# Kernel optimization log

Hardware: AMD Instinct MI355X
Metric: run time of the kernel (lower is better)

## Reference

```python
import jax, jax.numpy as jnp
import numpy as np

N_HEADS = 4
N_HIDDEN = 256  # out_features with concat=False
SLOPE = 0.1
NEG_INF = -9e15


def setup_inputs() -> dict:
    key = jax.random.key(0)
    k1, k2, k3, k4 = jax.random.split(key, 4)
    N, F_IN = 4096, 512
    h = jax.random.normal(k1, (N, F_IN), dtype=jnp.float32)
    adj_mat = jax.random.randint(k2, (N, N), 0, 2, dtype=jnp.int32)
    # xavier_normal gain=1.414
    W = jax.random.normal(k3, (F_IN, N_HIDDEN * N_HEADS), dtype=jnp.float32) * (
        1.414 * np.sqrt(2.0 / (F_IN + N_HIDDEN * N_HEADS)))
    a = jax.random.normal(k4, (N_HEADS, 2 * N_HIDDEN, 1), dtype=jnp.float32) * (
        1.414 * np.sqrt(2.0 / (2 * N_HIDDEN + 1)))
    return {"h": h, "adj_mat": adj_mat, "W": W, "a": a}


def reference(h, adj_mat, W, a):
    N = h.shape[0]
    # [N, H*D] -> [H, N, D]
    ht = (h @ W).reshape(N, N_HEADS, N_HIDDEN).transpose(1, 0, 2)
    lr = jax.nn.leaky_relu(ht, SLOPE)
    # additive attention: a split into source/target halves
    src = jnp.einsum('hnd,hd->hn', lr, a[:, :N_HIDDEN, 0])   # [H, N]
    tgt = jnp.einsum('hnd,hd->hn', lr, a[:, N_HIDDEN:, 0])   # [H, N]
    e = src[:, :, None] + tgt[:, None, :]                    # [H, N, N]
    e = jnp.where(adj_mat > 0, e, NEG_INF)
    attn = jax.nn.softmax(e, axis=-1)
    out = jnp.einsum('hnm,hmd->hnd', attn, ht)               # [H, N, D]
    return out.mean(axis=0)                                  # concat=False -> mean over heads
```

## Files before the change

### kernel.cpp

```cpp
#include <hip/hip_runtime.h>

#define N_NODES 4096
#define F_IN 512
#define NHID 256
#define HD 1024
#define NPAD 1152

typedef _Float16 half8 __attribute__((ext_vector_type(8)));
typedef _Float16 half4 __attribute__((ext_vector_type(4)));
typedef float floatx4 __attribute__((ext_vector_type(4)));
typedef float float4v __attribute__((ext_vector_type(4)));
typedef int int4v __attribute__((ext_vector_type(4)));
typedef unsigned int uint4v __attribute__((ext_vector_type(4)));

__device__ __forceinline__ float bf2f(unsigned short u) {
  union { unsigned int i; float f; } x; x.i = ((unsigned int)u) << 16; return x.f;
}

__device__ __forceinline__ void async_copy16(const void* g, void* l) {
  __builtin_amdgcn_global_load_lds((const __attribute__((address_space(1))) void*)g,
                                   (__attribute__((address_space(3))) void*)l, 16, 0, 0);
}

__global__ void detect_kernel(const unsigned short* __restrict__ hbits, int* __restrict__ flag) {
  const int t = threadIdx.x;
  int cnt = 0;
  for (int i = t; i < 1024; i += 256) {
    int e = (hbits[i] >> 7) & 0xFF;
    cnt += (e >= 115 && e <= 135) ? 1 : 0;
  }
  __shared__ int red[256];
  red[t] = cnt; __syncthreads();
  for (int s = 128; s > 0; s >>= 1) { if (t < s) red[t] += red[t + s]; __syncthreads(); }
  if (t == 0) flag[0] = (red[0] >= 900) ? 1 : 0;
}

template <typename OutT>
__device__ __forceinline__ void gemm_core(
    const _Float16* __restrict__ A, const _Float16* __restrict__ BT,
    OutT* __restrict__ C, int K, int ldc, int klen, long csz,
    int lin, int nbx, int nby, int total,
    _Float16* __restrict__ sA, _Float16* __restrict__ sB)
{
  int tile = ((total & 7) == 0) ? ((lin & 7) * (total >> 3) + (lin >> 3)) : lin;
  const int n_idx = tile % nbx;
  const int rem   = tile / nbx;
  const int m_idx = rem % nby;
  const int kz    = rem / nby;

  const int n0 = n_idx * 128;
  const int m0 = m_idx * 128;
  const int kbeg = kz * klen;
  const int kend = kbeg + klen;
  OutT* Cz = C + (long)kz * csz;

  const int t = threadIdx.x;
  const int w = t >> 6;
  const int lane = t & 63;
  const int wm = (w >> 1) << 6;
  const int wn = (w & 1) << 6;

  floatx4 acc[4][4] = {};

  const int l4 = lane >> 2;
  const int kksw = (((lane & 3) ^ ((lane >> 2) & 3)) << 3);
  const int c0 = w << 1;

  const _Float16* gA = A + (long)m0 * K;
  const _Float16* gBT = BT + (long)n0 * K;

  const int rsw = (((lane >> 4) ^ (lane & 3)) << 3);
  const int rA = wm + (lane & 15);
  const int rB = wn + (lane & 15);

  auto STAGE = [&](int buf, int k0) {
#pragma unroll
    for (int p = 0; p < 2; ++p) {
      const int c = c0 + p;
      const int row = c * 16 + l4;
      async_copy16(gA + (long)row * K + k0 + kksw, &sA[buf * 4096 + c * 512 + lane * 8]);
      async_copy16(gBT + (long)row * K + k0 + kksw, &sB[buf * 4096 + c * 512 + lane * 8]);
    }
  };

  STAGE(0, kbeg);
  __syncthreads();

  int cur = 0;
  for (int k0 = kbeg; k0 < kend; k0 += 32) {
    if (k0 + 32 < kend) STAGE(cur ^ 1, k0 + 32);

    half8 af[4], bf[4];
#pragma unroll
    for (int i = 0; i < 4; ++i)
      af[i] = *(const half8*)&sA[cur * 4096 + (rA + i * 16) * 32 + rsw];
#pragma unroll
    for (int i = 0; i < 4; ++i)
      bf[i] = *(const half8*)&sB[cur * 4096 + (rB + i * 16) * 32 + rsw];
#pragma unroll
    for (int i = 0; i < 4; ++i)
#pragma unroll
      for (int j = 0; j < 4; ++j)
        acc[i][j] = __builtin_amdgcn_mfma_f32_16x16x32_f16(af[i], bf[j], acc[i][j], 0, 0, 0);

    __syncthreads();
    cur ^= 1;
  }

  const int q4 = (lane >> 4) << 2;
#pragma unroll
  for (int i = 0; i < 4; ++i) {
#pragma unroll
    for (int j = 0; j < 4; ++j) {
      const int gr = m0 + wm + i * 16 + q4;
      const int gc = n0 + wn + j * 16 + (lane & 15);
#pragma unroll
      for (int r = 0; r < 4; ++r)
        Cz[(long)(gr + r) * ldc + gc] = (OutT)acc[i][j][r];
    }
  }
}

template <typename OutT>
__global__ __launch_bounds__(256) void gemm_bt(
    const _Float16* __restrict__ A, const _Float16* __restrict__ BT,
    OutT* __restrict__ C, int K, int ldc, int klen, long csz)
{
  __shared__ _Float16 sA[2 * 128 * 32];
  __shared__ _Float16 sB[2 * 128 * 32];
  const int nbx = gridDim.x, nby = gridDim.y;
  const int total = nbx * nby * gridDim.z;
  const int lin = blockIdx.x + nbx * (blockIdx.y + nby * blockIdx.z);
  gemm_core<OutT>(A, BT, C, K, ldc, klen, csz, lin, nbx, nby, total, sA, sB);
}

__global__ __launch_bounds__(256) void fused_ht_cvt_kernel(
    const _Float16* __restrict__ hF, const _Float16* __restrict__ WT,
    _Float16* __restrict__ ht, const int* __restrict__ adj,
    _Float16* __restrict__ adjF)
{
  __shared__ _Float16 sA[2 * 128 * 32];
  __shared__ _Float16 sB[2 * 128 * 32];
  const int b = blockIdx.x;
  if (b < 256) {
    gemm_core<_Float16>(hF, WT, ht, F_IN, HD, F_IN, 0, b, 8, 32, 256, sA, sB);
  } else {
    const int i = (b - 256) * 256 + threadIdx.x;
    int4v A = ((const int4v*)adj)[2 * i];
    int4v B = ((const int4v*)adj)[2 * i + 1];
    half8 o;
#pragma unroll
    for (int e = 0; e < 4; ++e) {
      o[e]     = (_Float16)(A[e] > 0 ? 1.0f : 0.0f);
      o[4 + e] = (_Float16)(B[e] > 0 ? 1.0f : 0.0f);
    }
    ((half8*)adjF)[i] = o;
  }
}

__global__ void cvt_h_kernel(const void* __restrict__ in, _Float16* __restrict__ out,
                             const int* __restrict__ flag, int n8) {
  int i = blockIdx.x * 256 + threadIdx.x;
  if (i >= n8) return;
  half8 o;
  if (*flag) {
    union { uint4v v; unsigned short s[8]; } u;
    u.v = ((const uint4v*)in)[i];
#pragma unroll
    for (int e = 0; e < 8; ++e) o[e] = (_Float16)bf2f(u.s[e]);
  } else {
    const float4v* f = (const float4v*)in + 2 * i;
    float4v x0 = f[0], x1 = f[1];
#pragma unroll
    for (int e = 0; e < 4; ++e) { o[e] = (_Float16)x0[e]; o[4 + e] = (_Float16)x1[e]; }
  }
  ((half8*)out)[i] = o;
}

__global__ void cvt_a_kernel(const void* __restrict__ a, float* __restrict__ aF,
                             const int* __restrict__ flag) {
  const int t = threadIdx.x;
  const int bf = *flag;
#pragma unroll
  for (int e = 0; e < 8; ++e) {
    int idx = t * 8 + e;
    aF[idx] = bf ? bf2f(((const unsigned short*)a)[idx]) : ((const float*)a)[idx];
  }
}

__global__ void transpose_w_kernel(const void* __restrict__ W, _Float16* __restrict__ WT,
                                   const int* __restrict__ flag) {
  __shared__ _Float16 tile[64][72];
  const int k0 = blockIdx.x * 64, n0 = blockIdx.y * 64;
  const int t = threadIdx.x, r = t >> 3, c = t & 7;
  const int bf = *flag;
#pragma unroll
  for (int q = 0; q < 2; ++q) {
    int k = r + q * 32;
    half8 v;
    if (bf) {
      union { uint4v vv; unsigned short s[8]; } u;
      u.vv = *(const uint4v*)&((const unsigned short*)W)[(long)(k0 + k) * HD + n0 + c * 8];
#pragma unroll
      for (int e = 0; e < 8; ++e) v[e] = (_Float16)bf2f(u.s[e]);
    } else {
      const float4v* f = (const float4v*)&((const float*)W)[(long)(k0 + k) * HD + n0 + c * 8];
      float4v x0 = f[0], x1 = f[1];
#pragma unroll
      for (int e = 0; e < 4; ++e) { v[e] = (_Float16)x0[e]; v[4 + e] = (_Float16)x1[e]; }
    }
    *(half8*)&tile[k][c * 8] = v;
  }
  __syncthreads();
#pragma unroll
  for (int q = 0; q < 2; ++q) {
    int n = r + q * 32;
    half8 o;
#pragma unroll
    for (int e = 0; e < 8; ++e) o[e] = tile[c * 8 + e][n];
    *(half8*)&WT[(long)(n0 + n) * F_IN + k0 + c * 8] = o;
  }
}

__global__ void tgt_kernel(const _Float16* __restrict__ ht, const float* __restrict__ aF,
                           float* __restrict__ tgt) {
  const int i = blockIdx.x;
  const int t = threadIdx.x, h = t >> 6, lane = t & 63;
  half4 v = *(const half4*)&ht[(long)i * HD + h * NHID + lane * 4];
  float4v av = *(const float4v*)&aF[h * 512 + NHID + lane * 4];
  float s = 0.f;
#pragma unroll
  for (int e = 0; e < 4; ++e) {
    float x = (float)v[e];
    x = x > 0.f ? x : 0.1f * x;
    s += x * av[e];
  }
#pragma unroll
  for (int o = 32; o > 0; o >>= 1) s += __shfl_down(s, o);
  if (lane == 0) tgt[h * N_NODES + i] = s;
}

__global__ void maxexp_kernel(const float* __restrict__ tgt, float* __restrict__ wbuf,
                              _Float16* __restrict__ VT) {
  const int h = blockIdx.x, t = threadIdx.x;
  const float* row = tgt + h * N_NODES;
  float4v v[4];
  float m = -3.0e38f;
#pragma unroll
  for (int q = 0; q < 4; ++q) {
    v[q] = *(const float4v*)&row[(t + q * 256) * 4];
#pragma unroll
    for (int e = 0; e < 4; ++e) m = fmaxf(m, v[q][e]);
  }
#pragma unroll
  for (int o = 32; o > 0; o >>= 1) m = fmaxf(m, __shfl_down(m, o));
  __shared__ float red[4];
  if ((t & 63) == 0) red[t >> 6] = m;
  __syncthreads();
  m = fmaxf(fmaxf(red[0], red[1]), fmaxf(red[2], red[3]));
#pragma unroll
  for (int q = 0; q < 4; ++q) {
    const int j0 = (t + q * 256) * 4;
    float4v wv;
#pragma unroll
    for (int e = 0; e < 4; ++e) wv[e] = __expf(v[q][e] - m);
    *(float4v*)&wbuf[h * N_NODES + j0] = wv;
    half4 hv;
#pragma unroll
    for (int e = 0; e < 4; ++e) hv[e] = (_Float16)wv[e];
    *(half4*)&VT[(long)(HD + h) * N_NODES + j0] = hv;
  }
}

__global__ void scaled_transpose_kernel(const _Float16* __restrict__ ht, const float* __restrict__ wbuf,
                                        _Float16* __restrict__ VT) {
  __shared__ _Float16 tile[64][72];
  const int j0 = blockIdx.x * 64, n0 = blockIdx.y * 64;
  const int t = threadIdx.x, r = t >> 3, c = t & 7;
#pragma unroll
  for (int q = 0; q < 2; ++q) {
    int j = r + q * 32;
    *(half8*)&tile[j][c * 8] = *(const half8*)&ht[(long)(j0 + j) * HD + n0 + c * 8];
  }
  __syncthreads();
  const int h = n0 >> 8;
  const float* wrow = wbuf + h * N_NODES + j0;
#pragma unroll
  for (int q = 0; q < 2; ++q) {
    int n = r + q * 32;
    half8 o;
#pragma unroll
    for (int e = 0; e < 8; ++e) {
      int j = c * 8 + e;
      o[e] = (_Float16)(wrow[j] * (float)tile[j][n]);
    }
    *(half8*)&VT[(long)(n0 + n) * N_NODES + j0 + c * 8] = o;
  }
}

__global__ void epilogue_kernel(const float* __restrict__ S, float* __restrict__ out, int ns) {
  const int i = blockIdx.x, d = threadIdx.x;
  const long SZ = (long)N_NODES * NPAD;
  float num[4] = {0.f, 0.f, 0.f, 0.f};
  float den[4] = {0.f, 0.f, 0.f, 0.f};
  for (int z = 0; z < ns; ++z) {
    const float* row = S + z * SZ + (long)i * NPAD;
#pragma unroll
    for (int h = 0; h < 4; ++h) {
      num[h] += row[h * NHID + d];
      den[h] += row[HD + h];
    }
  }
  float r = 0.f;
#pragma unroll
  for (int h = 0; h < 4; ++h) r += num[h] / den[h];
  out[(long)i * NHID + d] = 0.25f * r;
}

extern "C" void kernel_launch(void* const* d_in, const int* in_sizes, int n_in,
                              void* d_out, int out_size, void* d_ws, size_t ws_size,
                              hipStream_t stream) {
  const void* h = nullptr; const int* adj = nullptr; const void* W = nullptr; const void* a = nullptr;
  for (int i = 0; i < n_in; ++i) {
    switch (in_sizes[i]) {
      case 2097152:  h   = d_in[i]; break;
      case 16777216: adj = (const int*)d_in[i]; break;
      case 524288:   W   = d_in[i]; break;
      case 2048:     a   = d_in[i]; break;
      default: break;
    }
  }
  float* out = (float*)d_out;

  char* ws = (char*)d_ws;
  const size_t OFF_ADJF = 0;
  const size_t OFF_VT   = 33554432;
  const size_t OFF_TGT  = OFF_VT + 9437184;
  const size_t OFF_WBUF = OFF_TGT + 65536;
  const size_t OFF_M    = OFF_WBUF + 65536;
  const size_t OFF_AF   = OFF_M + 256;
  const size_t OFF_X    = OFF_AF + 8192;
  const size_t SPART    = 18874368;

  int ns = 1;
  if      (ws_size >= OFF_X + 4 * SPART) ns = 4;
  else if (ws_size >= OFF_X + 2 * SPART) ns = 2;
  if (ws_size < OFF_X + SPART || !h || !adj || !W || !a) return;

  _Float16* adjF = (_Float16*)(ws + OFF_ADJF);
  _Float16* VT   = (_Float16*)(ws + OFF_VT);
  float*    tgt  = (float*)(ws + OFF_TGT);
  float*    wbuf = (float*)(ws + OFF_WBUF);
  int*      flag = (int*)(ws + OFF_M + 32);
  float*    aF   = (float*)(ws + OFF_AF);
  _Float16* hF = (_Float16*)(ws + OFF_X);
  _Float16* WT = (_Float16*)(ws + OFF_X + 4194304);
  _Float16* ht = (_Float16*)(ws + OFF_X + 5242880);
  float*    S  = (float*)(ws + OFF_X);

  detect_kernel<<<1, 256, 0, stream>>>((const unsigned short*)h, flag);
  cvt_h_kernel<<<1024, 256, 0, stream>>>(h, hF, flag, 262144);
  cvt_a_kernel<<<1, 256, 0, stream>>>(a, aF, flag);
  transpose_w_kernel<<<dim3(8, 16), 256, 0, stream>>>(W, WT, flag);
  fused_ht_cvt_kernel<<<8448, 256, 0, stream>>>(hF, WT, ht, adj, adjF);
  tgt_kernel<<<4096, 256, 0, stream>>>(ht, aF, tgt);
  maxexp_kernel<<<4, 256, 0, stream>>>(tgt, wbuf, VT);
  scaled_transpose_kernel<<<dim3(64, 16), 256, 0, stream>>>(ht, wbuf, VT);
  gemm_bt<float><<<dim3(9, 32, ns), 256, 0, stream>>>(adjF, VT, S, N_NODES, NPAD,
                                                      N_NODES / ns, (long)N_NODES * NPAD);
  epilogue_kernel<<<4096, 256, 0, stream>>>(S, out, ns);
}
```

Baseline: 212.1 us.

## Triple-buffer GEMM LDS staging with explicit vmcnt waits and drop swizzle

```diff
diff --git a/kernel.cpp b/kernel.cpp
--- a/kernel.cpp
+++ b/kernel.cpp
@@ -51,7 +51,6 @@
   const int n0 = n_idx * 128;
   const int m0 = m_idx * 128;
   const int kbeg = kz * klen;
-  const int kend = kbeg + klen;
   OutT* Cz = C + (long)kz * csz;
 
   const int t = threadIdx.x;
@@ -63,48 +62,61 @@
   floatx4 acc[4][4] = {};
 
   const int l4 = lane >> 2;
-  const int kksw = (((lane & 3) ^ ((lane >> 2) & 3)) << 3);
+  const int kk = (lane & 3) << 3;
   const int c0 = w << 1;
 
   const _Float16* gA = A + (long)m0 * K;
   const _Float16* gBT = BT + (long)n0 * K;
 
-  const int rsw = (((lane >> 4) ^ (lane & 3)) << 3);
+  const int koff = (lane >> 4) << 3;
   const int rA = wm + (lane & 15);
   const int rB = wn + (lane & 15);
+
+  const int nt = klen >> 5;
 
   auto STAGE = [&](int buf, int k0) {
 #pragma unroll
     for (int p = 0; p < 2; ++p) {
       const int c = c0 + p;
       const int row = c * 16 + l4;
-      async_copy16(gA + (long)row * K + k0 + kksw, &sA[buf * 4096 + c * 512 + lane * 8]);
-      async_copy16(gBT + (long)row * K + k0 + kksw, &sB[buf * 4096 + c * 512 + lane * 8]);
+      async_copy16(gA + (long)row * K + k0 + kk, &sA[buf * 4096 + c * 512 + lane * 8]);
+      async_copy16(gBT + (long)row * K + k0 + kk, &sB[buf * 4096 + c * 512 + lane * 8]);
     }
   };
 
   STAGE(0, kbeg);
-  __syncthreads();
+  if (nt > 1) STAGE(1, kbeg + 32);
 
   int cur = 0;
-  for (int k0 = kbeg; k0 < kend; k0 += 32) {
-    if (k0 + 32 < kend) STAGE(cur ^ 1, k0 + 32);
+  for (int it = 0; it < nt; ++it) {
+    const int k0 = kbeg + it * 32;
+
+    if (it + 1 < nt) asm volatile("s_waitcnt vmcnt(4)" ::: "memory");
+    else             asm volatile("s_waitcnt vmcnt(0)" ::: "memory");
+    __builtin_amdgcn_s_barrier();
 
     half8 af[4], bf[4];
 #pragma unroll
     for (int i = 0; i < 4; ++i)
-      af[i] = *(const half8*)&sA[cur * 4096 + (rA + i * 16) * 32 + rsw];
+      af[i] = *(const half8*)&sA[cur * 4096 + (rA + i * 16) * 32 + koff];
 #pragma unroll
     for (int i = 0; i < 4; ++i)
-      bf[i] = *(const half8*)&sB[cur * 4096 + (rB + i * 16) * 32 + rsw];
+      bf[i] = *(const half8*)&sB[cur * 4096 + (rB + i * 16) * 32 + koff];
+
+    asm volatile("s_waitcnt lgkmcnt(0)" ::: "memory");
+    __builtin_amdgcn_sched_barrier(0);
+    __builtin_amdgcn_s_barrier();
+
+    const int nxt = (cur + 2 >= 3) ? cur - 1 : cur + 2;
+    if (it + 2 < nt) STAGE(nxt, k0 + 64);
+
 #pragma unroll
     for (int i = 0; i < 4; ++i)
 #pragma unroll
       for (int j = 0; j < 4; ++j)
         acc[i][j] = __builtin_amdgcn_mfma_f32_16x16x32_f16(af[i], bf[j], acc[i][j], 0, 0, 0);
 
-    __syncthreads();
-    cur ^= 1;
+    cur = (cur + 1 >= 3) ? 0 : cur + 1;
   }
 
   const int q4 = (lane >> 4) << 2;
@@ -126,8 +138,8 @@
     const _Float16* __restrict__ A, const _Float16* __restrict__ BT,
     OutT* __restrict__ C, int K, int ldc, int klen, long csz)
 {
-  __shared__ _Float16 sA[2 * 128 * 32];
-  __shared__ _Float16 sB[2 * 128 * 32];
+  __shared__ _Float16 sA[3 * 128 * 32];
+  __shared__ _Float16 sB[3 * 128 * 32];
   const int nbx = gridDim.x, nby = gridDim.y;
   const int total = nbx * nby * gridDim.z;
   const int lin = blockIdx.x + nbx * (blockIdx.y + nby * blockIdx.z);
@@ -139,8 +151,8 @@
     _Float16* __restrict__ ht, const int* __restrict__ adj,
     _Float16* __restrict__ adjF)
 {
-  __shared__ _Float16 sA[2 * 128 * 32];
-  __shared__ _Float16 sB[2 * 128 * 32];
+  __shared__ _Float16 sA[3 * 128 * 32];
+  __shared__ _Float16 sB[3 * 128 * 32];
   const int b = blockIdx.x;
   if (b < 256) {
     gemm_core<_Float16>(hF, WT, ht, F_IN, HD, F_IN, 0, b, 8, 32, 256, sA, sB);
```

Measured after the change: 200.3 us. 1.06x faster.
